# Kernel tuning notes

Hardware: AMD Instinct MI355X
Metric: run time of the kernel (lower is better)

The kernel has to match this reference:

```python
import jax, jax.numpy as jnp
import numpy as np

B, C, H, W = 8, 256, 32, 32
N_HEADS, N_GROUPS = 8, 4
HC = C // N_HEADS      # head channels = 32
GC = C // N_GROUPS     # group channels = 64
OFFSET_RANGE_FACTOR = 4.0


def dwconv3x3(x, w, b):
    # depthwise 3x3, stride 1, pad 1; x (B,Cc,H,W), w (Cc,1,3,3)
    y = jax.lax.conv_general_dilated(x, w, (1, 1), ((1, 1), (1, 1)),
                                     dimension_numbers=('NCHW', 'OIHW', 'NCHW'),
                                     feature_group_count=x.shape[1])
    return y + b[None, :, None, None]


def grid_sample_bilinear(img, pos_yx):
    # torch F.grid_sample, mode=bilinear, align_corners=True, padding_mode=zeros
    # img (BG,Cc,Hi,Wi); pos_yx (BG,Hs,Ws,2) in [-1,1], (y,x) order
    BG, Cc, Hi, Wi = img.shape
    Hs, Ws = pos_yx.shape[1], pos_yx.shape[2]
    y = (pos_yx[..., 0] + 1.0) * 0.5 * (Hi - 1)
    x = (pos_yx[..., 1] + 1.0) * 0.5 * (Wi - 1)
    y0 = jnp.floor(y); x0 = jnp.floor(x)
    yw = y - y0; xw = x - x0
    y0i = y0.astype(jnp.int32); x0i = x0.astype(jnp.int32)
    imgf = img.reshape(BG, Cc, Hi * Wi)

    def gather(yi, xi, wgt):
        valid = ((yi >= 0) & (yi < Hi) & (xi >= 0) & (xi < Wi)).astype(img.dtype)
        idx = jnp.clip(yi, 0, Hi - 1) * Wi + jnp.clip(xi, 0, Wi - 1)
        idx = jnp.broadcast_to(idx.reshape(BG, 1, Hs * Ws), (BG, Cc, Hs * Ws))
        vals = jnp.take_along_axis(imgf, idx, axis=2)
        return vals * (wgt * valid).reshape(BG, 1, Hs * Ws)

    out = (gather(y0i,     x0i,     (1 - yw) * (1 - xw))
         + gather(y0i,     x0i + 1, (1 - yw) * xw)
         + gather(y0i + 1, x0i,     yw * (1 - xw))
         + gather(y0i + 1, x0i + 1, yw * xw))
    return out.reshape(BG, Cc, Hs, Ws)


def setup_inputs() -> dict:
    key = jax.random.key(0)
    ks = jax.random.split(key, 16)
    s = 0.02
    return {
        'x': jax.random.normal(ks[0], (B, C, H, W), jnp.float32),
        'Wq': jax.random.normal(ks[1], (C, C), jnp.float32) * s,
        'bq': jax.random.normal(ks[2], (C,), jnp.float32) * s,
        'Wk': jax.random.normal(ks[3], (C, C), jnp.float32) * s,
        'bk': jax.random.normal(ks[4], (C,), jnp.float32) * s,
        'Wv': jax.random.normal(ks[5], (C, C), jnp.float32) * s,
        'bv': jax.random.normal(ks[6], (C,), jnp.float32) * s,
        'Wo': jax.random.normal(ks[7], (C, C), jnp.float32) * s,
        'bo': jax.random.normal(ks[8], (C,), jnp.float32) * s,
        'off_dw_w': jax.random.normal(ks[9], (GC, 1, 3, 3), jnp.float32) * s,
        'off_dw_b': jax.random.normal(ks[10], (GC,), jnp.float32) * s,
        'off_ln_g': jnp.ones((GC,), jnp.float32),
        'off_ln_b': jnp.zeros((GC,), jnp.float32),
        'off_pw_w': jax.random.normal(ks[11], (2, GC), jnp.float32) * s,
        'rpe_dw_w': jax.random.normal(ks[12], (C, 1, 3, 3), jnp.float32) * s,
        'rpe_dw_b': jax.random.normal(ks[13], (C,), jnp.float32) * s,
    }


def reference(x, Wq, bq, Wk, bk, Wv, bv, Wo, bo,
              off_dw_w, off_dw_b, off_ln_g, off_ln_b, off_pw_w,
              rpe_dw_w, rpe_dw_b):
    scale = HC ** -0.5
    # q projection (1x1 conv)
    q = jnp.einsum('oc,bchw->bohw', Wq, x) + bq[None, :, None, None]
    # offset prediction per group
    q_off = q.reshape(B * N_GROUPS, GC, H, W)
    o = dwconv3x3(q_off, off_dw_w, off_dw_b)
    mu = o.mean(axis=1, keepdims=True)
    var = ((o - mu) ** 2).mean(axis=1, keepdims=True)
    o = (o - mu) / jnp.sqrt(var + 1e-5) * off_ln_g[None, :, None, None] + off_ln_b[None, :, None, None]
    o = jax.nn.gelu(o, approximate=False)
    offset = jnp.einsum('oc,bchw->bohw', off_pw_w, o)  # (BG,2,Hk,Wk)
    Hk, Wk_ = offset.shape[2], offset.shape[3]
    n = Hk * Wk_
    offset_range = jnp.array([1.0 / (Hk - 1.0), 1.0 / (Wk_ - 1.0)], x.dtype).reshape(1, 2, 1, 1)
    offset = jnp.tanh(offset) * offset_range * OFFSET_RANGE_FACTOR
    offset = offset.transpose(0, 2, 3, 1)  # (BG,Hk,Wk,2) (y,x)
    ry = (jnp.linspace(0.5, Hk - 0.5, Hk, dtype=x.dtype) / (Hk - 1.0)) * 2.0 - 1.0
    rx = (jnp.linspace(0.5, Wk_ - 0.5, Wk_, dtype=x.dtype) / (Wk_ - 1.0)) * 2.0 - 1.0
    ref = jnp.stack(jnp.meshgrid(ry, rx, indexing='ij'), axis=-1)[None]  # (1,Hk,Wk,2)
    pos = offset + ref  # offset_range_factor >= 0: no clamp
    # irregular bilinear gather
    x_sampled = grid_sample_bilinear(x.reshape(B * N_GROUPS, GC, H, W), pos)
    x_sampled = x_sampled.reshape(B, C, n)
    # k/v projections on sampled points
    qf = q.reshape(B * N_HEADS, HC, H * W)
    k = (jnp.einsum('oc,bcn->bon', Wk, x_sampled) + bk[None, :, None]).reshape(B * N_HEADS, HC, n)
    v = (jnp.einsum('oc,bcn->bon', Wv, x_sampled) + bv[None, :, None]).reshape(B * N_HEADS, HC, n)
    attn = jnp.einsum('bcm,bcn->bmn', qf, k) * scale
    # dwc_pe residual positional encoding
    lepe = dwconv3x3(qf.reshape(B, C, H, W), rpe_dw_w, rpe_dw_b).reshape(B * N_HEADS, HC, H * W)
    attn = jax.nn.softmax(attn, axis=2)
    out = jnp.einsum('bmn,bcn->bcm', attn, v) + lepe
    out = out.reshape(B, C, H, W)
    y = jnp.einsum('oc,bchw->bohw', Wo, out) + bo[None, :, None, None]
    return y
```

## Files before the change

kernel.cpp:

```cpp
#include <hip/hip_runtime.h>
#include <math.h>


#define NPOS 1024

typedef float f32x4   __attribute__((ext_vector_type(4)));
typedef short bf16x8  __attribute__((ext_vector_type(8)));
typedef short short4v __attribute__((ext_vector_type(4)));
typedef unsigned uint4v __attribute__((ext_vector_type(4)));

__device__ __forceinline__ short f2bf(float f) {
    unsigned u = __float_as_uint(f);
    unsigned r = (u + 0x7FFFu + ((u >> 16) & 1u)) >> 16;
    return (short)r;
}
__device__ __forceinline__ float bf2f(short s) {
    return __uint_as_float(((unsigned)(unsigned short)s) << 16);
}
__device__ __forceinline__ unsigned cvtpk(float a, float b) {
    unsigned r;
    asm("v_cvt_pk_bf16_f32 %0, %1, %2" : "=v"(r) : "v"(a), "v"(b));
    return r;
}

__device__ __forceinline__ bf16x8 ldfrag(const short* base, int row, int KE,
                                         int s0, int s1, int swz) {
    const short* r = base + row * KE;
    short4v lo = *(const short4v*)(r + ((s0 ^ swz) << 2));
    short4v hi = *(const short4v*)(r + ((s1 ^ swz) << 2));
    bf16x8 f = {lo[0], lo[1], lo[2], lo[3], hi[0], hi[1], hi[2], hi[3]};
    return f;
}

__device__ __forceinline__ bf16x8 gfrag(const short* __restrict__ r, int g) {
    short4v lo = *(const short4v*)(r + 4 * g);
    short4v hi = *(const short4v*)(r + 16 + 4 * g);
    bf16x8 f = {lo[0], lo[1], lo[2], lo[3], hi[0], hi[1], hi[2], hi[3]};
    return f;
}

__device__ __forceinline__ void stpair(short* base, int row, int KE, int h, int swz,
                                       bf16x8 v8) {
    short4v lo = {v8[0], v8[1], v8[2], v8[3]};
    short4v hi = {v8[4], v8[5], v8[6], v8[7]};
    *(short4v*)(base + row * KE + (((2 * h) ^ swz) << 2)) = lo;
    *(short4v*)(base + row * KE + (((2 * h + 1) ^ swz) << 2)) = hi;
}

__global__ __launch_bounds__(256) void transpose_x(const float* __restrict__ x,
    short* __restrict__ xT,
    const float* __restrict__ Wq, const float* __restrict__ Wk,
    const float* __restrict__ Wv, const float* __restrict__ Wo,
    short* __restrict__ Wb)
{
    const int t = threadIdx.x;
    if (blockIdx.z == 8) {
        int gid = (blockIdx.y * 16 + blockIdx.x) * 256 + t;
        #pragma unroll
        for (int i = 0; i < 16; ++i) {
            int idx = gid + i * 16384;
            const float* src = (idx < 65536) ? Wq : (idx < 131072) ? Wk
                             : (idx < 196608) ? Wv : Wo;
            Wb[idx] = f2bf(src[idx & 65535]);
        }
        return;
    }
    __shared__ float tile[64][69];
    const int p0 = blockIdx.x * 64, c0 = blockIdx.y * 64, b = blockIdx.z;
    #pragma unroll
    for (int i = 0; i < 4; ++i) {
        int id = t + i * 256;
        int row = id >> 4, q = id & 15;
        float4 v = *(const float4*)(x + ((long)(b * 256 + c0 + row)) * NPOS + p0 + q * 4);
        tile[row][q * 4 + 0] = v.x; tile[row][q * 4 + 1] = v.y;
        tile[row][q * 4 + 2] = v.z; tile[row][q * 4 + 3] = v.w;
    }
    __syncthreads();
    #pragma unroll
    for (int i = 0; i < 2; ++i) {
        int id = t + i * 256;
        int p = id >> 3, cg = id & 7;
        bf16x8 o;
        #pragma unroll
        for (int j = 0; j < 8; ++j) o[j] = f2bf(tile[cg * 8 + j][p]);
        *(bf16x8*)(xT + ((long)(b * 1024 + p0 + p)) * 256 + c0 + cg * 8) = o;
    }
}

template<int MODE>
__global__ __launch_bounds__(256) void gemm_mfma(
    const short* __restrict__ A, const short* __restrict__ Bt,
    const float* __restrict__ bias,
    float* __restrict__ outF, short* __restrict__ outT)
{
    __shared__ short As[2][64 * 64];
    __shared__ short Bs[2][64 * 64];
    const int t = threadIdx.x;
    const int n0 = blockIdx.x * 64, m0 = blockIdx.y * 64;
    const int b = blockIdx.z;
    const int lane = t & 63, w = t >> 6;
    const int wm = w >> 1, wn = w & 1;
    const int l15 = lane & 15, g = lane >> 4;
    const int srow = t >> 3, sp = t & 7;
    f32x4 z = {0.f, 0.f, 0.f, 0.f};
    f32x4 acc[2][2];
    acc[0][0] = z; acc[0][1] = z; acc[1][0] = z; acc[1][1] = z;

    bf16x8 ar[2], br[2];
    #pragma unroll
    for (int i = 0; i < 2; ++i) {
        int row = srow + i * 32;
        ar[i] = *(const bf16x8*)(A + (long)(m0 + row) * 256 + sp * 8);
        br[i] = *(const bf16x8*)(Bt + ((long)b * 1024 + n0 + row) * 256 + sp * 8);
        stpair(As[0], row, 64, sp, row & 15, ar[i]);
        stpair(Bs[0], row, 64, sp, row & 15, br[i]);
    }
    __syncthreads();

    for (int kt = 0; kt < 4; ++kt) {
        const int cur = kt & 1;
        if (kt < 3) {
            const int k0 = (kt + 1) * 64;
            #pragma unroll
            for (int i = 0; i < 2; ++i) {
                int row = srow + i * 32;
                ar[i] = *(const bf16x8*)(A + (long)(m0 + row) * 256 + k0 + sp * 8);
                br[i] = *(const bf16x8*)(Bt + ((long)b * 1024 + n0 + row) * 256 + k0 + sp * 8);
            }
        }
        #pragma unroll
        for (int kk = 0; kk < 2; ++kk) {
            bf16x8 af[2], bfr[2];
            #pragma unroll
            for (int mi = 0; mi < 2; ++mi) {
                int row = wm * 32 + mi * 16 + l15;
                af[mi] = ldfrag(As[cur], row, 64, kk * 8 + g, kk * 8 + 4 + g, row & 15);
            }
            #pragma unroll
            for (int ni = 0; ni < 2; ++ni) {
                int row = wn * 32 + ni * 16 + l15;
                bfr[ni] = ldfrag(Bs[cur], row, 64, kk * 8 + g, kk * 8 + 4 + g, row & 15);
            }
            __builtin_amdgcn_s_setprio(1);
            #pragma unroll
            for (int mi = 0; mi < 2; ++mi)
                #pragma unroll
                for (int ni = 0; ni < 2; ++ni)
                    acc[mi][ni] = __builtin_amdgcn_mfma_f32_16x16x32_bf16(
                        af[mi], bfr[ni], acc[mi][ni], 0, 0, 0);
            __builtin_amdgcn_s_setprio(0);
        }
        if (kt < 3) {
            #pragma unroll
            for (int i = 0; i < 2; ++i) {
                int row = srow + i * 32;
                stpair(As[cur ^ 1], row, 64, sp, row & 15, ar[i]);
                stpair(Bs[cur ^ 1], row, 64, sp, row & 15, br[i]);
            }
        }
        __syncthreads();
    }
    #pragma unroll
    for (int mi = 0; mi < 2; ++mi) {
        const int mbase = m0 + wm * 32 + mi * 16 + g * 4;
        float bv[4];
        #pragma unroll
        for (int j = 0; j < 4; ++j) bv[j] = bias[mbase + j];
        #pragma unroll
        for (int ni = 0; ni < 2; ++ni) {
            const int n = n0 + wn * 32 + ni * 16 + l15;
            f32x4 r = acc[mi][ni];
            #pragma unroll
            for (int j = 0; j < 4; ++j) r[j] += bv[j];
            #pragma unroll
            for (int j = 0; j < 4; ++j)
                outF[((long)b * 256 + mbase + j) * NPOS + n] = r[j];
            if constexpr (MODE == 0) {
                const float sc = 0.25503486f;
                short4v p = {f2bf(r[0] * sc), f2bf(r[1] * sc),
                             f2bf(r[2] * sc), f2bf(r[3] * sc)};
                int bh = b * 8 + (mbase >> 5);
                *(short4v*)(outT + ((long)bh * 1024 + n) * 32 + (mbase & 31)) = p;
            }
        }
    }
}

__global__ __launch_bounds__(256) void gemm_kv(
    const short* __restrict__ Ak, const short* __restrict__ Av,
    const short* __restrict__ Bt,
    const float* __restrict__ bk, const float* __restrict__ bv,
    short* __restrict__ kT, short* __restrict__ vN)
{
    __shared__ short Ks[2][64 * 64];
    __shared__ short Vs[2][64 * 64];
    __shared__ short Bs[2][64 * 64];
    const int t = threadIdx.x;
    const int n0 = blockIdx.x * 64, m0 = blockIdx.y * 64;
    const int b = blockIdx.z;
    const int lane = t & 63, w = t >> 6;
    const int wm = w >> 1, wn = w & 1;
    const int l15 = lane & 15, g = lane >> 4;
    const int srow = t >> 3, sp = t & 7;
    f32x4 z = {0.f, 0.f, 0.f, 0.f};
    f32x4 acck[2][2], accv[2][2];
    acck[0][0] = z; acck[0][1] = z; acck[1][0] = z; acck[1][1] = z;
    accv[0][0] = z; accv[0][1] = z; accv[1][0] = z; accv[1][1] = z;

    bf16x8 a1[2], a2[2], bb[2];
    #pragma unroll
    for (int i = 0; i < 2; ++i) {
        int row = srow + i * 32;
        a1[i] = *(const bf16x8*)(Ak + (long)(m0 + row) * 256 + sp * 8);
        a2[i] = *(const bf16x8*)(Av + (long)(m0 + row) * 256 + sp * 8);
        bb[i] = *(const bf16x8*)(Bt + ((long)b * 1024 + n0 + row) * 256 + sp * 8);
        stpair(Ks[0], row, 64, sp, row & 15, a1[i]);
        stpair(Vs[0], row, 64, sp, row & 15, a2[i]);
        stpair(Bs[0], row, 64, sp, row & 15, bb[i]);
    }
    __syncthreads();

    for (int kt = 0; kt < 4; ++kt) {
        const int cur = kt & 1;
        if (kt < 3) {
            const int k0 = (kt + 1) * 64;
            #pragma unroll
            for (int i = 0; i < 2; ++i) {
                int row = srow + i * 32;
                a1[i] = *(const bf16x8*)(Ak + (long)(m0 + row) * 256 + k0 + sp * 8);
                a2[i] = *(const bf16x8*)(Av + (long)(m0 + row) * 256 + k0 + sp * 8);
                bb[i] = *(const bf16x8*)(Bt + ((long)b * 1024 + n0 + row) * 256 + k0 + sp * 8);
            }
        }
        #pragma unroll
        for (int kk = 0; kk < 2; ++kk) {
            bf16x8 afk[2], afv[2], bfr[2];
            #pragma unroll
            for (int mi = 0; mi < 2; ++mi) {
                int row = wm * 32 + mi * 16 + l15;
                afk[mi] = ldfrag(Ks[cur], row, 64, kk * 8 + g, kk * 8 + 4 + g, row & 15);
                afv[mi] = ldfrag(Vs[cur], row, 64, kk * 8 + g, kk * 8 + 4 + g, row & 15);
            }
            #pragma unroll
            for (int ni = 0; ni < 2; ++ni) {
                int row = wn * 32 + ni * 16 + l15;
                bfr[ni] = ldfrag(Bs[cur], row, 64, kk * 8 + g, kk * 8 + 4 + g, row & 15);
            }
            __builtin_amdgcn_s_setprio(1);
            #pragma unroll
            for (int mi = 0; mi < 2; ++mi)
                #pragma unroll
                for (int ni = 0; ni < 2; ++ni) {
                    acck[mi][ni] = __builtin_amdgcn_mfma_f32_16x16x32_bf16(
                        afk[mi], bfr[ni], acck[mi][ni], 0, 0, 0);
                    accv[mi][ni] = __builtin_amdgcn_mfma_f32_16x16x32_bf16(
                        afv[mi], bfr[ni], accv[mi][ni], 0, 0, 0);
                }
            __builtin_amdgcn_s_setprio(0);
        }
        if (kt < 3) {
            #pragma unroll
            for (int i = 0; i < 2; ++i) {
                int row = srow + i * 32;
                stpair(Ks[cur ^ 1], row, 64, sp, row & 15, a1[i]);
                stpair(Vs[cur ^ 1], row, 64, sp, row & 15, a2[i]);
                stpair(Bs[cur ^ 1], row, 64, sp, row & 15, bb[i]);
            }
        }
        __syncthreads();
    }
    #pragma unroll
    for (int mi = 0; mi < 2; ++mi) {
        const int mbase = m0 + wm * 32 + mi * 16 + g * 4;
        float bk4[4], bv4[4];
        #pragma unroll
        for (int j = 0; j < 4; ++j) { bk4[j] = bk[mbase + j]; bv4[j] = bv[mbase + j]; }
        #pragma unroll
        for (int ni = 0; ni < 2; ++ni) {
            const int n = n0 + wn * 32 + ni * 16 + l15;
            f32x4 rk = acck[mi][ni], rv = accv[mi][ni];
            short4v pk = {f2bf(rk[0] + bk4[0]), f2bf(rk[1] + bk4[1]),
                          f2bf(rk[2] + bk4[2]), f2bf(rk[3] + bk4[3])};
            int bh = b * 8 + (mbase >> 5);
            *(short4v*)(kT + ((long)bh * 1024 + n) * 32 + (mbase & 31)) = pk;
            #pragma unroll
            for (int j = 0; j < 4; ++j)
                vN[((long)b * 256 + mbase + j) * NPOS + n] = f2bf(rv[j] + bv4[j]);
        }
    }
}

__global__ __launch_bounds__(256) void offset_sample(
    const float* __restrict__ q, const short* __restrict__ xT,
    const float* __restrict__ dww, const float* __restrict__ dwb,
    const float* __restrict__ lng, const float* __restrict__ lnb,
    const float* __restrict__ pww, short* __restrict__ xsT)
{
    __shared__ float q3[64][3][33];
    __shared__ float wS[576];
    __shared__ float bS[64], gS[64], lbS[64], pS[128];
    const int t = threadIdx.x;
    const int y = blockIdx.x, bg = blockIdx.y;
    const float* qb = q + (long)bg * 64 * NPOS;
    for (int i = t; i < 576; i += 256) wS[i] = dww[i];
    if (t < 64) { bS[t] = dwb[t]; gS[t] = lng[t]; lbS[t] = lnb[t]; }
    else if (t >= 128 && t < 256) pS[t - 128] = pww[t - 128];
    #pragma unroll
    for (int i = 0; i < 6; ++i) {
        int id = t + i * 256;
        int c = id / 24, rx = id - c * 24;
        int r = rx >> 3, q4 = (rx & 7) * 4;
        int yy = y + r - 1;
        float4 v = make_float4(0.f, 0.f, 0.f, 0.f);
        if (yy >= 0 && yy < 32)
            v = *(const float4*)(qb + (long)c * NPOS + yy * 32 + q4);
        q3[c][r][q4 + 0] = v.x; q3[c][r][q4 + 1] = v.y;
        q3[c][r][q4 + 2] = v.z; q3[c][r][q4 + 3] = v.w;
    }
    __syncthreads();
    const int p = t >> 3, cg = t & 7;
    float oc[8];
    float s = 0.f, s2 = 0.f;
    #pragma unroll
    for (int j = 0; j < 8; ++j) {
        int c = cg * 8 + j;
        float acc = bS[c];
        #pragma unroll
        for (int dy = 0; dy < 3; ++dy)
            #pragma unroll
            for (int dx = 0; dx < 3; ++dx) {
                int xx = p + dx - 1;
                if (xx >= 0 && xx < 32)
                    acc += wS[c * 9 + dy * 3 + dx] * q3[c][dy][xx];
            }
        oc[j] = acc;
        s += acc; s2 += acc * acc;
    }
    s  += __shfl_xor(s, 1);  s  += __shfl_xor(s, 2);  s  += __shfl_xor(s, 4);
    s2 += __shfl_xor(s2, 1); s2 += __shfl_xor(s2, 2); s2 += __shfl_xor(s2, 4);
    float mu = s * 0.015625f;
    float var = s2 * 0.015625f - mu * mu;
    float rstd = rsqrtf(var + 1e-5f);
    float a0 = 0.f, a1 = 0.f;
    #pragma unroll
    for (int j = 0; j < 8; ++j) {
        int c = cg * 8 + j;
        float on = (oc[j] - mu) * rstd * gS[c] + lbS[c];
        float ge = 0.5f * on * (1.f + erff(on * 0.70710678118654752f));
        a0 += pS[c] * ge;
        a1 += pS[64 + c] * ge;
    }
    a0 += __shfl_xor(a0, 1); a0 += __shfl_xor(a0, 2); a0 += __shfl_xor(a0, 4);
    a1 += __shfl_xor(a1, 1); a1 += __shfl_xor(a1, 2); a1 += __shfl_xor(a1, 4);
    const float rng = 4.f / 31.f;
    float py = tanhf(a0) * rng + ((y + 0.5f) / 31.f) * 2.f - 1.f;
    float px = tanhf(a1) * rng + ((p + 0.5f) / 31.f) * 2.f - 1.f;
    float fy = (py + 1.f) * 15.5f;
    float fx = (px + 1.f) * 15.5f;
    float y0f = floorf(fy), x0f = floorf(fx);
    int y0 = (int)y0f, x0 = (int)x0f;
    float yw = fy - y0f, xw = fx - x0f;
    const short* base = xT + ((long)(bg >> 2) * 1024) * 256 + (bg & 3) * 64 + cg * 8;
    float acc8[8] = {};
    #pragma unroll
    for (int cy = 0; cy < 2; ++cy)
        #pragma unroll
        for (int cx = 0; cx < 2; ++cx) {
            int yi = y0 + cy, xi = x0 + cx;
            float wg = (cy ? yw : 1.f - yw) * (cx ? xw : 1.f - xw);
            if (yi >= 0 && yi < 32 && xi >= 0 && xi < 32) {
                bf16x8 v8 = *(const bf16x8*)(base + (long)(yi * 32 + xi) * 256);
                #pragma unroll
                for (int j = 0; j < 8; ++j) acc8[j] += wg * bf2f(v8[j]);
            }
        }
    bf16x8 o;
    #pragma unroll
    for (int j = 0; j < 8; ++j) o[j] = f2bf(acc8[j]);
    *(bf16x8*)(xsT + ((long)(bg >> 2) * 1024 + y * 32 + p) * 256 + (bg & 3) * 64 + cg * 8) = o;
}

__global__ __launch_bounds__(512, 4) void attn_mfma(
    const short* __restrict__ qT, const short* __restrict__ kT,
    const short* __restrict__ vN, const float* __restrict__ qf,
    const float* __restrict__ rdw, const float* __restrict__ rdb,
    short* __restrict__ aoutT)
{
    __shared__ short kS[2][2][64 * 32];
    __shared__ short vS[2][2][32 * 64];
    __shared__ float oT[128 * 33];
    __shared__ short qr[6][32][33];
    __shared__ float wR[288], bR[32], Lb[2][128];
    const int t = threadIdx.x;
    const int bid = blockIdx.x;
    const int bh = (bid & 7) * 8 + ((bid >> 3) & 7);
    const int mt = bid >> 6;
    const int m0 = mt * 128;
    const int lane = t & 63, w = t >> 6;
    const int g2 = w >> 2, gw = w & 3;
    const int l15 = lane & 15, g = lane >> 4;
    const long base32 = (long)bh * 32768;
    const int c0 = (bh & 7) * 32;
    const int tg = t & 255;
    const int krow_ = tg >> 2, kh = tg & 3;
    const int vc = tg >> 3, vh = tg & 7;
    const int nbase = g2 * 512;
    f32x4 z = {0.f, 0.f, 0.f, 0.f};

    {
        const int y0 = (m0 >> 5) - 1;
        #pragma unroll
        for (int i = 0; i < 3; ++i) {
            int id = t + i * 512;
            int xq = id & 7, cc = (id >> 3) & 31, r = id >> 8;
            int yy = y0 + r;
            float4 v = make_float4(0.f, 0.f, 0.f, 0.f);
            if (yy >= 0 && yy < 32)
                v = *(const float4*)(qf + base32 + (long)cc * NPOS + yy * 32 + xq * 4);
            qr[r][cc][xq * 4 + 0] = f2bf(v.x); qr[r][cc][xq * 4 + 1] = f2bf(v.y);
            qr[r][cc][xq * 4 + 2] = f2bf(v.z); qr[r][cc][xq * 4 + 3] = f2bf(v.w);
        }
        if (t < 32) bR[t] = rdb[c0 + t];
        for (int i = t; i < 288; i += 512) wR[i] = rdw[c0 * 9 + i];
    }

    int qrow[2]; bf16x8 qb[2];
    #pragma unroll
    for (int f = 0; f < 2; ++f) {
        qrow[f] = gw * 32 + f * 16 + l15;
        qb[f] = gfrag(qT + base32 + (long)(m0 + qrow[f]) * 32, g);
    }

    bf16x8 kr = *(const bf16x8*)(kT + base32 + (long)(nbase + krow_) * 32 + kh * 8);
    bf16x8 vr = *(const bf16x8*)(vN + base32 + (long)vc * NPOS + nbase + vh * 8);
    stpair(kS[g2][0], krow_, 32, kh, (krow_ >> 1) & 7, kr);
    stpair(vS[g2][0], vc, 64, vh, vc & 15, vr);
    __syncthreads();

    f32x4 Lacc[2]; Lacc[0] = z; Lacc[1] = z;
    f32x4 po[2][2];
    po[0][0] = z; po[0][1] = z; po[1][0] = z; po[1][1] = z;

    for (int it = 0; it < 8; ++it) {
        const int cur = it & 1;
        if (it < 7) {
            const int n0n = nbase + (it + 1) * 64;
            kr = *(const bf16x8*)(kT + base32 + (long)(n0n + krow_) * 32 + kh * 8);
            vr = *(const bf16x8*)(vN + base32 + (long)vc * NPOS + n0n + vh * 8);
        }
        bf16x8 ka[4];
        #pragma unroll
        for (int j = 0; j < 4; ++j) {
            int kr2 = j * 16 + l15;
            ka[j] = ldfrag(kS[g2][cur], kr2, 32, g, 4 + g, (kr2 >> 1) & 7);
        }
        f32x4 s[2][4];
        #pragma unroll
        for (int f = 0; f < 2; ++f)
            #pragma unroll
            for (int j = 0; j < 4; ++j)
                s[f][j] = __builtin_amdgcn_mfma_f32_16x16x32_bf16(ka[j], qb[f], z, 0, 0, 0);
        #pragma unroll
        for (int f = 0; f < 2; ++f)
            #pragma unroll
            for (int j = 0; j < 4; ++j) {
                #pragma unroll
                for (int r = 0; r < 4; ++r) s[f][j][r] = exp2f(s[f][j][r]);
                Lacc[f] += s[f][j];
            }
        bf16x8 pb[2][2];
        #pragma unroll
        for (int f = 0; f < 2; ++f)
            #pragma unroll
            for (int ks = 0; ks < 2; ++ks) {
                uint4v u;
                u[0] = cvtpk(s[f][2 * ks][0], s[f][2 * ks][1]);
                u[1] = cvtpk(s[f][2 * ks][2], s[f][2 * ks][3]);
                u[2] = cvtpk(s[f][2 * ks + 1][0], s[f][2 * ks + 1][1]);
                u[3] = cvtpk(s[f][2 * ks + 1][2], s[f][2 * ks + 1][3]);
                pb[f][ks] = __builtin_bit_cast(bf16x8, u);
            }
        #pragma unroll
        for (int cs = 0; cs < 2; ++cs) {
            int vrow = cs * 16 + l15;
            #pragma unroll
            for (int ks = 0; ks < 2; ++ks) {
                bf16x8 va = ldfrag(vS[g2][cur], vrow, 64, ks * 8 + g, ks * 8 + 4 + g, vrow & 15);
                #pragma unroll
                for (int f = 0; f < 2; ++f)
                    po[cs][f] = __builtin_amdgcn_mfma_f32_16x16x32_bf16(
                        va, pb[f][ks], po[cs][f], 0, 0, 0);
            }
        }
        if (it < 7) {
            stpair(kS[g2][cur ^ 1], krow_, 32, kh, (krow_ >> 1) & 7, kr);
            stpair(vS[g2][cur ^ 1], vc, 64, vh, vc & 15, vr);
        }
        __syncthreads();
    }
    #pragma unroll
    for (int f = 0; f < 2; ++f) {
        float ls = Lacc[f][0] + Lacc[f][1] + Lacc[f][2] + Lacc[f][3];
        ls += __shfl_xor(ls, 16);
        ls += __shfl_xor(ls, 32);
        if (lane < 16) Lb[g2][gw * 32 + f * 16 + lane] = ls;
    }
    if (g2 == 0) {
        #pragma unroll
        for (int cs = 0; cs < 2; ++cs)
            #pragma unroll
            for (int f = 0; f < 2; ++f)
                #pragma unroll
                for (int r = 0; r < 4; ++r)
                    oT[qrow[f] * 33 + cs * 16 + g * 4 + r] = po[cs][f][r];
    }
    __syncthreads();
    if (g2 == 1) {
        #pragma unroll
        for (int cs = 0; cs < 2; ++cs)
            #pragma unroll
            for (int f = 0; f < 2; ++f)
                #pragma unroll
                for (int r = 0; r < 4; ++r)
                    oT[qrow[f] * 33 + cs * 16 + g * 4 + r] += po[cs][f][r];
    }
    __syncthreads();
    #pragma unroll
    for (int i = 0; i < 8; ++i) {
        int idx = t + i * 512;
        int c = idx & 31, m = idx >> 5;
        int ml = m >> 5, xx0 = m & 31;
        float inv = 1.f / (Lb[0][m] + Lb[1][m]);
        float acc = 0.f;
        #pragma unroll
        for (int dy = 0; dy < 3; ++dy)
            #pragma unroll
            for (int dx = 0; dx < 3; ++dx) {
                int xx = xx0 + dx - 1;
                if (xx >= 0 && xx < 32)
                    acc += wR[c * 9 + dy * 3 + dx] * bf2f(qr[ml + dy][c][xx]);
            }
        float v = oT[m * 33 + c] * inv + acc + bR[c];
        aoutT[(((long)(bh >> 3)) * 1024 + m0 + m) * 256 + (bh & 7) * 32 + c] = f2bf(v);
    }
}

extern "C" void kernel_launch(void* const* d_in, const int* in_sizes, int n_in,
                              void* d_out, int out_size, void* d_ws, size_t ws_size,
                              hipStream_t stream)
{
    const float* x   = (const float*)d_in[0];
    const float* Wq  = (const float*)d_in[1];
    const float* bq  = (const float*)d_in[2];
    const float* Wk  = (const float*)d_in[3];
    const float* bk  = (const float*)d_in[4];
    const float* Wv  = (const float*)d_in[5];
    const float* bv  = (const float*)d_in[6];
    const float* Wo  = (const float*)d_in[7];
    const float* bo  = (const float*)d_in[8];
    const float* odw = (const float*)d_in[9];
    const float* odb = (const float*)d_in[10];
    const float* olg = (const float*)d_in[11];
    const float* olb = (const float*)d_in[12];
    const float* opw = (const float*)d_in[13];
    const float* rdw = (const float*)d_in[14];
    const float* rdb = (const float*)d_in[15];

    float* ws = (float*)d_ws;
    const size_t SZ = (size_t)2097152;
    float* qf  = ws;
    short* sb  = (short*)(ws + SZ);
    short* Wb  = sb;
    short* xT  = Wb + 262144;
    short* xsT = xT + SZ;
    short* qTb = xsT + SZ;
    short* kTb = qTb + SZ;
    short* vNb = kTb + SZ;
    float* y   = (float*)d_out;
    short* aoT = xsT;

    dim3 gg(16, 4, 8), gg9(16, 4, 9);
    transpose_x<<<gg9, 256, 0, stream>>>(x, xT, Wq, Wk, Wv, Wo, Wb);
    gemm_mfma<0><<<gg, 256, 0, stream>>>(Wb, xT, bq, qf, qTb);
    offset_sample<<<dim3(32, 32), 256, 0, stream>>>(qf, xT, odw, odb, olg, olb, opw, xsT);
    gemm_kv<<<gg, 256, 0, stream>>>(Wb + 65536, Wb + 131072, xsT, bk, bv, kTb, vNb);
    attn_mfma<<<512, 512, 0, stream>>>(qTb, kTb, vNb, qf, rdw, rdb, aoT);
    gemm_mfma<3><<<gg, 256, 0, stream>>>(Wb + 196608, aoT, bo, y, nullptr);
}
```

Measured before the change: 74.20 us.

## Drop fp32 q buffer, read bf16 scaled qT in consumers; XCD-aware block remap

The Q projection no longer writes a full fp32 q tensor. The offset-sampling and attention kernels now rebuild q from the bf16 pre-scaled qT buffer by multiplying by the inverse scale, which cuts global writes and reads of an 8 MB intermediate. The GEMM kernels also switch to a 1D grid with a block-index remap that places neighbouring n-tiles on the same XCD, aiming for better L2 reuse. In exchange, the offset conv/LayerNorm path and the LePE path now use bf16-rounded q, which lowers precision.

```diff
diff --git a/kernel.cpp b/kernel.cpp
--- a/kernel.cpp
+++ b/kernel.cpp
@@ -96,8 +96,11 @@
     __shared__ short As[2][64 * 64];
     __shared__ short Bs[2][64 * 64];
     const int t = threadIdx.x;
-    const int n0 = blockIdx.x * 64, m0 = blockIdx.y * 64;
-    const int b = blockIdx.z;
+    const int bid = blockIdx.x;
+    const int xcd = bid & 7, rest = bid >> 3;
+    const int n0 = (xcd * 2 + (rest & 1)) * 64;
+    const int m0 = ((rest >> 1) & 3) * 64;
+    const int b  = rest >> 3;
     const int lane = t & 63, w = t >> 6;
     const int wm = w >> 1, wn = w & 1;
     const int l15 = lane & 15, g = lane >> 4;
@@ -172,9 +175,11 @@
             f32x4 r = acc[mi][ni];
             #pragma unroll
             for (int j = 0; j < 4; ++j) r[j] += bv[j];
-            #pragma unroll
-            for (int j = 0; j < 4; ++j)
-                outF[((long)b * 256 + mbase + j) * NPOS + n] = r[j];
+            if constexpr (MODE == 3) {
+                #pragma unroll
+                for (int j = 0; j < 4; ++j)
+                    outF[((long)b * 256 + mbase + j) * NPOS + n] = r[j];
+            }
             if constexpr (MODE == 0) {
                 const float sc = 0.25503486f;
                 short4v p = {f2bf(r[0] * sc), f2bf(r[1] * sc),
@@ -196,8 +201,11 @@
     __shared__ short Vs[2][64 * 64];
     __shared__ short Bs[2][64 * 64];
     const int t = threadIdx.x;
-    const int n0 = blockIdx.x * 64, m0 = blockIdx.y * 64;
-    const int b = blockIdx.z;
+    const int bid = blockIdx.x;
+    const int xcd = bid & 7, rest = bid >> 3;
+    const int n0 = (xcd * 2 + (rest & 1)) * 64;
+    const int m0 = ((rest >> 1) & 3) * 64;
+    const int b  = rest >> 3;
     const int lane = t & 63, w = t >> 6;
     const int wm = w >> 1, wn = w & 1;
     const int l15 = lane & 15, g = lane >> 4;
@@ -291,7 +299,7 @@
 }
 
 __global__ __launch_bounds__(256) void offset_sample(
-    const float* __restrict__ q, const short* __restrict__ xT,
+    const short* __restrict__ qTv, const short* __restrict__ xT,
     const float* __restrict__ dww, const float* __restrict__ dwb,
     const float* __restrict__ lng, const float* __restrict__ lnb,
     const float* __restrict__ pww, short* __restrict__ xsT)
@@ -301,21 +309,23 @@
     __shared__ float bS[64], gS[64], lbS[64], pS[128];
     const int t = threadIdx.x;
     const int y = blockIdx.x, bg = blockIdx.y;
-    const float* qb = q + (long)bg * 64 * NPOS;
+    const float inv_sc = 1.0f / 0.25503486f;
     for (int i = t; i < 576; i += 256) wS[i] = dww[i];
     if (t < 64) { bS[t] = dwb[t]; gS[t] = lng[t]; lbS[t] = lnb[t]; }
     else if (t >= 128 && t < 256) pS[t - 128] = pww[t - 128];
-    #pragma unroll
-    for (int i = 0; i < 6; ++i) {
-        int id = t + i * 256;
-        int c = id / 24, rx = id - c * 24;
-        int r = rx >> 3, q4 = (rx & 7) * 4;
-        int yy = y + r - 1;
-        float4 v = make_float4(0.f, 0.f, 0.f, 0.f);
-        if (yy >= 0 && yy < 32)
-            v = *(const float4*)(qb + (long)c * NPOS + yy * 32 + q4);
-        q3[c][r][q4 + 0] = v.x; q3[c][r][q4 + 1] = v.y;
-        q3[c][r][q4 + 2] = v.z; q3[c][r][q4 + 3] = v.w;
+    {
+        const int o = t >> 5, xx = t & 31;
+        const int bh = (bg >> 2) * 8 + (bg & 3) * 2 + (o >> 2);
+        const int ho = (o & 3) * 8;
+        #pragma unroll
+        for (int r = 0; r < 3; ++r) {
+            int yy = y + r - 1;
+            bf16x8 v8 = {0, 0, 0, 0, 0, 0, 0, 0};
+            if (yy >= 0 && yy < 32)
+                v8 = *(const bf16x8*)(qTv + ((long)bh * 1024 + yy * 32 + xx) * 32 + ho);
+            #pragma unroll
+            for (int j = 0; j < 8; ++j) q3[o * 8 + j][r][xx] = bf2f(v8[j]) * inv_sc;
+        }
     }
     __syncthreads();
     const int p = t >> 3, cg = t & 7;
@@ -382,7 +392,7 @@
 
 __global__ __launch_bounds__(512, 4) void attn_mfma(
     const short* __restrict__ qT, const short* __restrict__ kT,
-    const short* __restrict__ vN, const float* __restrict__ qf,
+    const short* __restrict__ vN,
     const float* __restrict__ rdw, const float* __restrict__ rdb,
     short* __restrict__ aoutT)
 {
@@ -409,16 +419,20 @@
 
     {
         const int y0 = (m0 >> 5) - 1;
-        #pragma unroll
-        for (int i = 0; i < 3; ++i) {
+        const float inv_sc = 1.0f / 0.25503486f;
+        #pragma unroll
+        for (int i = 0; i < 2; ++i) {
             int id = t + i * 512;
-            int xq = id & 7, cc = (id >> 3) & 31, r = id >> 8;
-            int yy = y0 + r;
-            float4 v = make_float4(0.f, 0.f, 0.f, 0.f);
-            if (yy >= 0 && yy < 32)
-                v = *(const float4*)(qf + base32 + (long)cc * NPOS + yy * 32 + xq * 4);
-            qr[r][cc][xq * 4 + 0] = f2bf(v.x); qr[r][cc][xq * 4 + 1] = f2bf(v.y);
-            qr[r][cc][xq * 4 + 2] = f2bf(v.z); qr[r][cc][xq * 4 + 3] = f2bf(v.w);
+            if (id < 768) {
+                int r = id >> 7, o = (id >> 5) & 3, xx = id & 31;
+                int yy = y0 + r;
+                bf16x8 v8 = {0, 0, 0, 0, 0, 0, 0, 0};
+                if (yy >= 0 && yy < 32)
+                    v8 = *(const bf16x8*)(qT + base32 + (long)(yy * 32 + xx) * 32 + o * 8);
+                #pragma unroll
+                for (int j = 0; j < 8; ++j)
+                    qr[r][o * 8 + j][xx] = f2bf(bf2f(v8[j]) * inv_sc);
+            }
         }
         if (t < 32) bR[t] = rdb[c0 + t];
         for (int i = t; i < 288; i += 512) wR[i] = rdw[c0 * 9 + i];
@@ -566,10 +580,8 @@
     const float* rdw = (const float*)d_in[14];
     const float* rdb = (const float*)d_in[15];
 
-    float* ws = (float*)d_ws;
     const size_t SZ = (size_t)2097152;
-    float* qf  = ws;
-    short* sb  = (short*)(ws + SZ);
+    short* sb  = (short*)d_ws;
     short* Wb  = sb;
     short* xT  = Wb + 262144;
     short* xsT = xT + SZ;
@@ -579,11 +591,11 @@
     float* y   = (float*)d_out;
     short* aoT = xsT;
 
-    dim3 gg(16, 4, 8), gg9(16, 4, 9);
+    dim3 gg9(16, 4, 9);
     transpose_x<<<gg9, 256, 0, stream>>>(x, xT, Wq, Wk, Wv, Wo, Wb);
-    gemm_mfma<0><<<gg, 256, 0, stream>>>(Wb, xT, bq, qf, qTb);
-    offset_sample<<<dim3(32, 32), 256, 0, stream>>>(qf, xT, odw, odb, olg, olb, opw, xsT);
-    gemm_kv<<<gg, 256, 0, stream>>>(Wb + 65536, Wb + 131072, xsT, bk, bv, kTb, vNb);
-    attn_mfma<<<512, 512, 0, stream>>>(qTb, kTb, vNb, qf, rdw, rdb, aoT);
-    gemm_mfma<3><<<gg, 256, 0, stream>>>(Wb + 196608, aoT, bo, y, nullptr);
-}
+    gemm_mfma<0><<<512, 256, 0, stream>>>(Wb, xT, bq, nullptr, qTb);
+    offset_sample<<<dim3(32, 32), 256, 0, stream>>>(qTb, xT, odw, odb, olg, olb, opw, xsT);
+    gemm_kv<<<512, 256, 0, stream>>>(Wb + 65536, Wb + 131072, xsT, bk, bv, kTb, vNb);
+    attn_mfma<<<512, 512, 0, stream>>>(qTb, kTb, vNb, rdw, rdb, aoT);
+    gemm_mfma<3><<<512, 256, 0, stream>>>(Wb + 196608, aoT, bo, y, nullptr);
+}
```

Result: faster. 69.68 us (median of 2 runs) (-6.1%).
